# Performance work log

Measured on AMD Instinct MI355X. Metric: run time of the kernel, lower is better.

The kernel has to match this reference:

```python
import jax, jax.numpy as jnp
import numpy as np

N_NODES = 50000
N_EDGES = 800000
IN, HID, OUT = 128, 256, 128
BN_EPS = 1e-5

def setup_inputs() -> dict:
    key = jax.random.key(0)
    ks = jax.random.split(key, 16)
    def lin(k, fan_in, shape):
        b = 1.0 / np.sqrt(fan_in)
        return jax.random.uniform(k, shape, jnp.float32, -b, b)
    return {
        "node_feat": jax.random.normal(ks[0], (N_NODES, IN), jnp.float32),
        "coord_feat": jax.random.normal(ks[1], (N_NODES, 3), jnp.float32),
        "src": jax.random.randint(ks[2], (N_EDGES,), 0, N_NODES, jnp.int32),
        "dst": jax.random.randint(ks[3], (N_EDGES,), 0, N_NODES, jnp.int32),
        "W_e1": lin(ks[4], 2 * IN + 1, (2 * IN + 1, HID)),
        "b_e1": jnp.zeros((HID,), jnp.float32),
        "W_e2": lin(ks[5], HID, (HID, HID)),
        "b_e2": jnp.zeros((HID,), jnp.float32),
        "W_c1": lin(ks[6], HID, (HID, HID)),
        "b_c1": jnp.zeros((HID,), jnp.float32),
        "W_c2": lin(ks[7], HID, (HID, 1)),
        "W_n1": lin(ks[8], IN + HID, (IN + HID, HID)),
        "b_n1": jnp.zeros((HID,), jnp.float32),
        "W_n2": lin(ks[9], HID, (HID, OUT)),
        "b_n2": jnp.zeros((OUT,), jnp.float32),
        "gamma": jnp.ones((OUT,), jnp.float32),
        "beta": jnp.zeros((OUT,), jnp.float32),
    }

def reference(node_feat, coord_feat, src, dst, W_e1, b_e1, W_e2, b_e2,
              W_c1, b_c1, W_c2, W_n1, b_n1, W_n2, b_n2, gamma, beta):
    silu = jax.nn.silu
    # per-edge geometry (DGL u_sub_v: src - dst)
    x_diff = coord_feat[src] - coord_feat[dst]              # [E, 3]
    radial = jnp.sum(jnp.square(x_diff), axis=1, keepdims=True)  # [E, 1]
    x_diff = x_diff / (jnp.sqrt(radial) + 1e-30)
    # edge MLP on gathered features
    f = jnp.concatenate([node_feat[src], node_feat[dst], radial], axis=-1)  # [E, 2*IN+1]
    msg_h = silu(silu(f @ W_e1 + b_e1) @ W_e2 + b_e2)       # [E, HID]
    # coord message
    msg_x = (silu(msg_h @ W_c1 + b_c1) @ W_c2) * x_diff     # [E, 3]
    # aggregate at destination nodes
    h_neigh = jax.ops.segment_sum(msg_h, dst, num_segments=N_NODES)  # sum
    x_sum = jax.ops.segment_sum(msg_x, dst, num_segments=N_NODES)
    deg = jax.ops.segment_sum(jnp.ones((msg_x.shape[0],), msg_x.dtype), dst,
                              num_segments=N_NODES)
    x_neigh = x_sum / jnp.maximum(deg, 1.0)[:, None]        # mean; 0 for isolated nodes
    # node MLP + BatchNorm (training-mode batch stats, biased var)
    h = silu(jnp.concatenate([node_feat, h_neigh], axis=-1) @ W_n1 + b_n1) @ W_n2 + b_n2
    mu = jnp.mean(h, axis=0)
    var = jnp.mean(jnp.square(h - mu), axis=0)
    h = (h - mu) * jax.lax.rsqrt(var + BN_EPS) * gamma + beta
    x = coord_feat + x_neigh
    return h, x
```

## Files before the change

### kernel.cpp

```cpp
#include <hip/hip_runtime.h>
#include <stdint.h>

typedef unsigned short u16;
typedef __bf16 bf16x8 __attribute__((ext_vector_type(8)));
typedef unsigned short u16x8 __attribute__((ext_vector_type(8)));
typedef float f32x4 __attribute__((ext_vector_type(4)));

#define N_NODES 50000
#define N_EDGES 800000

enum : uint32_t {
  WS_WT_E1 = 0u,
  WS_WT_E2 = 131072u,
  WS_WT_C1 = 262144u,
  WS_WT_N1 = 393216u,
  WS_WT_N2 = 589824u,
  WS_WRAD  = 655360u,
  WS_WC2   = 656384u,
  WS_B_E1  = 657408u,
  WS_B_E2  = 658432u,
  WS_B_C1  = 659456u,
  WS_B_N1  = 660480u,
  WS_B_N2  = 661504u,
  WS_GAMMA = 662016u,
  WS_BETA  = 662528u,
  WS_SCALE = 663040u,
  WS_SHIFT = 663552u,
  WS_STAT  = 664064u,
  WS_FLAG  = 665600u,
  WS_DEG   = 1048576u,
  WS_OFF   = 1248576u,
  WS_BSUM  = 1448704u,
  WS_BPRE  = 1449728u,
  WS_CUR   = 1450752u,
  WS_EID   = 1650752u,
  WS_XSUM  = 4850752u,
  WS_CF    = 5450752u,
  WS_NF    = 6050752u,
  WS_HN    = 18850752u,
  WS_PA    = 70050752u,
  WS_PB    = 95675328u,
  WS_PRE_END = 121299904u
};

__device__ __forceinline__ float b2f(u16 u){ uint32_t x=((uint32_t)u)<<16; float f; __builtin_memcpy(&f,&x,4); return f; }
__device__ __forceinline__ u16 f2b(float f){ __bf16 h = (__bf16)f; return __builtin_bit_cast(unsigned short, h); }
__device__ __forceinline__ float silu_f(float x){
  return x * __builtin_amdgcn_rcpf(1.0f + __expf(-x));
}
__device__ __forceinline__ float ldin(const void* p, int i, int fl){
  return fl ? ((const float*)p)[i] : b2f(((const u16*)p)[i]);
}

__global__ void detect_k(const void* nf, int* flag){
  if (threadIdx.x == 0){
    const u16* p = (const u16*)nf;
    int cnt = 0;
    for (int i=0;i<128;i++){
      u16 u = p[2*i];
      int e = (u >> 7) & 0xFF;
      if (e >= 0x90) cnt++;
    }
    *flag = (cnt >= 8) ? 1 : 0;
  }
}

__global__ void cvt_nf_k(const void* nf, char* ws, const int* flagp){
  int fl = *flagp;
  int i = blockIdx.x*256 + threadIdx.x;
  if (i >= (N_NODES*128)/4) return;
  ushort4* out = (ushort4*)(ws + WS_NF);
  if (fl){
    const float4* p = (const float4*)nf;
    float4 v = p[i];
    ushort4 o; o.x=f2b(v.x); o.y=f2b(v.y); o.z=f2b(v.z); o.w=f2b(v.w);
    out[i] = o;
  } else {
    out[i] = ((const ushort4*)nf)[i];
  }
}

__global__ void cvt_cf_k(const void* cd, char* ws, const int* flagp){
  int fl = *flagp;
  int i = blockIdx.x*256 + threadIdx.x;
  if (i >= N_NODES*3) return;
  ((float*)(ws + WS_CF))[i] = ldin(cd, i, fl);
}

__global__ void prep_k(const void* We1, const void* be1, const void* We2, const void* be2,
                       const void* Wc1, const void* bc1, const void* Wc2,
                       const void* Wn1, const void* bn1, const void* Wn2, const void* bn2,
                       const void* gam, const void* bet, char* ws, const int* flagp)
{
  int fl = *flagp;
  int g = blockIdx.x*256 + threadIdx.x;
  if (g < 65536){ int n=g>>8,k=g&255; ((u16*)(ws+WS_WT_E1))[n*256+k]=f2b(ldin(We1,k*256+n,fl)); return; } g-=65536;
  if (g < 65536){
    int j=g&7, l=(g>>3)&63, nblk=(g>>9)&15, kk=g>>13;
    int n=nblk*16+(l&15), k=kk*32+((l>>4)&3)*8+j;
    ((u16*)(ws+WS_WT_E2))[g]=f2b(ldin(We2,k*256+n,fl)); return; } g-=65536;
  if (g < 65536){
    int j=g&7, l=(g>>3)&63, nblk=(g>>9)&15, kk=g>>13;
    int n=nblk*16+(l&15), k=kk*32+((l>>4)&3)*8+j;
    ((u16*)(ws+WS_WT_C1))[g]=f2b(ldin(Wc1,k*256+n,fl)); return; } g-=65536;
  if (g < 98304){ int n=g/384,k=g-n*384; ((u16*)(ws+WS_WT_N1))[n*384+k]=f2b(ldin(Wn1,k*256+n,fl)); return; } g-=98304;
  if (g < 32768){ int n=g>>8,k=g&255; ((u16*)(ws+WS_WT_N2))[n*256+k]=f2b(ldin(Wn2,k*128+n,fl)); return; } g-=32768;
  if (g < 256){ ((float*)(ws+WS_WRAD))[g]=ldin(We1,65536+g,fl); return; } g-=256;
  if (g < 256){ ((float*)(ws+WS_WC2))[g]=ldin(Wc2,g,fl); return; } g-=256;
  if (g < 256){ ((float*)(ws+WS_B_E1))[g]=ldin(be1,g,fl); return; } g-=256;
  if (g < 256){ ((float*)(ws+WS_B_E2))[g]=ldin(be2,g,fl); return; } g-=256;
  if (g < 256){ ((float*)(ws+WS_B_C1))[g]=ldin(bc1,g,fl); return; } g-=256;
  if (g < 256){ ((float*)(ws+WS_B_N1))[g]=ldin(bn1,g,fl); return; } g-=256;
  if (g < 128){ ((float*)(ws+WS_B_N2))[g]=ldin(bn2,g,fl); return; } g-=128;
  if (g < 128){ ((float*)(ws+WS_GAMMA))[g]=ldin(gam,g,fl); return; } g-=128;
  if (g < 128){ ((float*)(ws+WS_BETA))[g]=ldin(bet,g,fl); return; }
}

__global__ void histo_k(const int* __restrict__ dst, int* __restrict__ deg){
  int e = blockIdx.x*256 + threadIdx.x;
  if (e < N_EDGES) atomicAdd(&deg[dst[e]], 1);
}

__global__ void scanA_k(const int* __restrict__ deg, int* __restrict__ off, int* __restrict__ bsum){
  int t = threadIdx.x; int i = blockIdx.x*256 + t;
  int lane = t & 63, w = t >> 6;
  int v = (i < N_NODES) ? deg[i] : 0;
  int x = v;
  #pragma unroll
  for (int d=1; d<64; d<<=1){ int o = __shfl_up(x, d, 64); if (lane >= d) x += o; }
  __shared__ int wt[4];
  if (lane == 63) wt[w] = x;
  __syncthreads();
  int add = 0;
  if (w > 0) add += wt[0];
  if (w > 1) add += wt[1];
  if (w > 2) add += wt[2];
  x += add;
  if (i < N_NODES) off[i] = x;
  if (t == 255) bsum[blockIdx.x] = x;
}

__global__ void scanB_k(const int* __restrict__ bsum, int* __restrict__ bpre, int* __restrict__ off){
  int t = threadIdx.x;
  int lane = t & 63, w = t >> 6;
  int v = (t < 196) ? bsum[t] : 0;
  int x = v;
  #pragma unroll
  for (int d=1; d<64; d<<=1){ int o = __shfl_up(x, d, 64); if (lane >= d) x += o; }
  __shared__ int wt[4];
  if (lane == 63) wt[w] = x;
  __syncthreads();
  int add = 0;
  if (w > 0) add += wt[0];
  if (w > 1) add += wt[1];
  if (w > 2) add += wt[2];
  x += add;
  if (t < 196) bpre[t] = x - v;
  if (t == 255) off[N_NODES] = x;
}

__global__ void scanC_k(const int* __restrict__ deg, int* __restrict__ off,
                        const int* __restrict__ bpre, int* __restrict__ cur){
  int i = blockIdx.x*256 + threadIdx.x;
  if (i >= N_NODES) return;
  int excl = off[i] - deg[i] + bpre[blockIdx.x];
  off[i] = excl; cur[i] = excl;
}

__global__ void scatter_k(const int* __restrict__ dst, int* __restrict__ cur, int* __restrict__ eid){
  int e = blockIdx.x*256 + threadIdx.x;
  if (e >= N_EDGES) return;
  int p = atomicAdd(&cur[dst[e]], 1);
  eid[p] = e;
}

__global__ __launch_bounds__(512, 4) void pab_k(const u16* __restrict__ nfc,
                                                const char* __restrict__ wsw,
                                                u16* __restrict__ pa, u16* __restrict__ pb)
{
  const int t = threadIdx.x, lane = t & 63, wid = t >> 6;
  const int mw = wid & 1, nw = wid >> 1;
  const int mbase = mw << 5, nbase = nw << 6;
  const int l15 = lane & 15, l4 = lane >> 4;
  const int tile = blockIdx.x;
  const u16* Wt = (const u16*)(wsw + WS_WT_E1);
  const float* b1 = (const float*)(wsw + WS_B_E1);

  for (int sel = 0; sel < 2; ++sel){
    u16* out = sel ? pb : pa;
    f32x4 acc[2][4];
    #pragma unroll
    for (int mi=0;mi<2;mi++)
    #pragma unroll
    for (int ni=0;ni<4;ni++){ float b_ = sel ? 0.f : b1[nbase+ni*16+l15]; acc[mi][ni]=(f32x4){b_,b_,b_,b_}; }

    #pragma unroll
    for (int kk=0;kk<4;kk++){
      const int kel = kk*32 + l4*8;
      bf16x8 av[2];
      #pragma unroll
      for (int mi=0;mi<2;mi++){
        int row = tile*64 + mbase + mi*16 + l15;
        if (row >= N_NODES) row = 0;
        av[mi] = *(const bf16x8*)(nfc + (size_t)row*128 + kel);
      }
      #pragma unroll
      for (int ni=0;ni<4;ni++){
        int n_ = nbase + ni*16 + l15;
        bf16x8 bv = *(const bf16x8*)(Wt + (size_t)n_*256 + sel*128 + kel);
        #pragma unroll
        for (int mi=0;mi<2;mi++)
          acc[mi][ni] = __builtin_amdgcn_mfma_f32_16x16x32_bf16(av[mi], bv, acc[mi][ni], 0,0,0);
      }
    }
    #pragma unroll
    for (int mi=0;mi<2;mi++)
    #pragma unroll
    for (int ni=0;ni<4;ni++)
    #pragma unroll
    for (int j=0;j<4;j++){
      int m_ = tile*64 + mbase + mi*16 + l4*4 + j;
      if (m_ < N_NODES){
        int n_ = nbase + ni*16 + l15;
        out[(size_t)m_*256 + n_] = f2b(acc[mi][ni][j]);
      }
    }
  }
}

#define FRAG_GEMM2(FB, BIAS_L) do { \
  _Pragma("unroll") for (int mi=0;mi<2;mi++) _Pragma("unroll") for (int ni=0;ni<4;ni++){ \
    float b_ = BIAS_L[nbase + ni*16 + l15]; acc[mi][ni] = (f32x4){b_,b_,b_,b_}; } \
  bf16x8 bvc[4]; \
  _Pragma("unroll") for (int ni=0;ni<4;ni++) \
    bvc[ni] = *(const bf16x8*)(FB + (((nblk0 + ni)<<9)) + lane*8); \
  _Pragma("unroll") for (int kk=0;kk<8;kk++){ \
    const int kel = kk*32 + l4*8; \
    bf16x8 av[2]; \
    _Pragma("unroll") for (int mi=0;mi<2;mi++){ \
      int row = mbase + mi*16 + l15; \
      uint32_t byte = ((uint32_t)row<<9) ^ ((uint32_t)kel<<1) ^ ((uint32_t)(row&7)<<4); \
      av[mi] = *(const bf16x8*)((const char*)h_lds + byte); \
    } \
    bf16x8 bvn[4]; \
    if (kk < 7){ \
      _Pragma("unroll") for (int ni=0;ni<4;ni++) \
        bvn[ni] = *(const bf16x8*)(FB + ((((kk+1)<<4) + nblk0 + ni)<<9) + lane*8); \
    } \
    _Pragma("unroll") for (int ni=0;ni<4;ni++) \
    _Pragma("unroll") for (int mi=0;mi<2;mi++) \
      acc[mi][ni] = __builtin_amdgcn_mfma_f32_16x16x32_bf16(av[mi], bvc[ni], acc[mi][ni], 0,0,0); \
    if (kk < 7){ \
      _Pragma("unroll") for (int ni=0;ni<4;ni++) bvc[ni] = bvn[ni]; \
    } \
  } } while(0)

#define SILU_STORE2() do { \
  _Pragma("unroll") for (int mi=0;mi<2;mi++) _Pragma("unroll") for (int ni=0;ni<4;ni++) \
  _Pragma("unroll") for (int j=0;j<4;j++){ \
    int m_ = mbase + mi*16 + l4*4 + j; int n_ = nbase + ni*16 + l15; \
    float v_ = silu_f(acc[mi][ni][j]); \
    uint32_t byte = ((uint32_t)m_<<9) ^ ((uint32_t)n_<<1) ^ ((uint32_t)(m_&7)<<4); \
    *(u16*)((char*)h_lds + byte) = f2b(v_); \
  } } while(0)

template<bool PRE>
__global__ __launch_bounds__(512, 4) void edge_mlp(
    const u16* __restrict__ nfc, const float* __restrict__ coord,
    const int* __restrict__ src, const int* __restrict__ dst,
    const char* __restrict__ wsw, const int* __restrict__ eid,
    const u16* __restrict__ pa, const u16* __restrict__ pb,
    float* __restrict__ h_neigh, float* __restrict__ xsum)
{
  __shared__ u16 h_lds[16384];
  __shared__ int s_ids[64], d_ids[64];
  __shared__ float rad_l[64], xd_l[64][3];
  __shared__ float cpart[4][64];
  __shared__ float b1_l[256], b2_l[256], b3_l[256], wc2_l[256];

  const int t = threadIdx.x, lane = t & 63, wid = t >> 6;
  const int mw = wid & 1, nw = wid >> 1;
  const int mbase = mw << 5, nbase = nw << 6;
  const int nblk0 = nw << 2;
  const int l15 = lane & 15, l4 = lane >> 4;
  const int tile = blockIdx.x;

  const u16* FB2 = (const u16*)(wsw + WS_WT_E2);
  const u16* FB3 = (const u16*)(wsw + WS_WT_C1);

  if (t < 64) {
    int e = eid[tile*64 + t];
    int s = src[e], d = dst[e];
    s_ids[t] = s; d_ids[t] = d;
    float ax = coord[s*3+0]-coord[d*3+0];
    float ay = coord[s*3+1]-coord[d*3+1];
    float az = coord[s*3+2]-coord[d*3+2];
    float r2 = ax*ax+ay*ay+az*az;
    float inv = 1.0f/(sqrtf(r2) + 1e-30f);
    rad_l[t] = r2; xd_l[t][0]=ax*inv; xd_l[t][1]=ay*inv; xd_l[t][2]=az*inv;
  }
  if (t >= 64 && t < 320) {
    int c = t - 64;
    if constexpr (!PRE) b1_l[c] = ((const float*)(wsw+WS_B_E1))[c];
    b2_l[c]  = ((const float*)(wsw+WS_B_E2))[c];
    b3_l[c]  = ((const float*)(wsw+WS_B_C1))[c];
    wc2_l[c] = ((const float*)(wsw+WS_WC2))[c];
  }
  __syncthreads();

  f32x4 acc[2][4];

  if constexpr (PRE) {
    const int r1 = t >> 3, cq = (t & 7) << 5;
    const int s1 = s_ids[r1], d1 = d_ids[r1];
    const float rr = rad_l[r1];
    const u16* par = pa + (size_t)s1*256 + cq;
    const u16* pbr = pb + (size_t)d1*256 + cq;
    const float* wrg = (const float*)(wsw + WS_WRAD) + cq;
    u16x8 ua[4], ub[4];
    #pragma unroll
    for (int q=0;q<4;q++){ ua[q] = *(const u16x8*)(par + q*8); ub[q] = *(const u16x8*)(pbr + q*8); }
    #pragma unroll
    for (int q=0;q<4;q++){
      f32x4 w0 = *(const f32x4*)(wrg + q*8);
      f32x4 w1 = *(const f32x4*)(wrg + q*8 + 4);
      u16x8 o;
      #pragma unroll
      for (int j=0;j<8;j++){
        float wv = (j<4) ? w0[j] : w1[j-4];
        float hv = silu_f(b2f(ua[q][j]) + b2f(ub[q][j]) + rr*wv);
        o[j] = f2b(hv);
      }
      int c = cq + q*8;
      uint32_t byte = ((uint32_t)r1<<9) ^ ((uint32_t)c<<1) ^ ((uint32_t)(r1&7)<<4);
      *(u16x8*)((char*)h_lds + byte) = o;
    }
  } else {
    #pragma unroll
    for (int mi=0;mi<2;mi++)
    #pragma unroll
    for (int ni=0;ni<4;ni++){ float b_ = b1_l[nbase+ni*16+l15]; acc[mi][ni]=(f32x4){b_,b_,b_,b_}; }
    const u16* Wt1 = (const u16*)(wsw + WS_WT_E1);
    #pragma unroll
    for (int kk=0;kk<8;kk++){
      const int kel = kk*32 + l4*8;
      bf16x8 av[2];
      #pragma unroll
      for (int mi=0;mi<2;mi++){
        int row = mbase + mi*16 + l15;
        int nid = (kk < 4) ? s_ids[row] : d_ids[row];
        int k = (kk < 4) ? kel : (kel - 128);
        av[mi] = *(const bf16x8*)(nfc + (size_t)nid*128 + k);
      }
      #pragma unroll
      for (int ni=0;ni<4;ni++){
        int n_ = nbase + ni*16 + l15;
        bf16x8 bv = *(const bf16x8*)(Wt1 + (size_t)n_*256 + kel);
        #pragma unroll
        for (int mi=0;mi<2;mi++)
          acc[mi][ni] = __builtin_amdgcn_mfma_f32_16x16x32_bf16(av[mi], bv, acc[mi][ni], 0,0,0);
      }
    }
    #pragma unroll
    for (int mi=0;mi<2;mi++)
    #pragma unroll
    for (int ni=0;ni<4;ni++){
      int n_ = nbase + ni*16 + l15;
      float wrn = ((const float*)(wsw+WS_WRAD))[n_];
      #pragma unroll
      for (int j=0;j<4;j++){
        int m_ = mbase + mi*16 + l4*4 + j;
        float v_ = silu_f(acc[mi][ni][j] + rad_l[m_]*wrn);
        uint32_t byte = ((uint32_t)m_<<9) ^ ((uint32_t)n_<<1) ^ ((uint32_t)(m_&7)<<4);
        *(u16*)((char*)h_lds + byte) = f2b(v_);
      }
    }
  }
  __syncthreads();

  FRAG_GEMM2(FB2, b2_l);
  __syncthreads();
  SILU_STORE2();
  __syncthreads();

  FRAG_GEMM2(FB3, b3_l);
  float part[2][4];
  #pragma unroll
  for (int mi=0;mi<2;mi++)
  #pragma unroll
  for (int j=0;j<4;j++) part[mi][j] = 0.f;
  #pragma unroll
  for (int mi=0;mi<2;mi++)
  #pragma unroll
  for (int ni=0;ni<4;ni++){
    int n_ = nbase + ni*16 + l15;
    float w = wc2_l[n_];
    #pragma unroll
    for (int j=0;j<4;j++) part[mi][j] += silu_f(acc[mi][ni][j]) * w;
  }
  #pragma unroll
  for (int off_=1; off_<16; off_<<=1)
  #pragma unroll
  for (int mi=0;mi<2;mi++)
  #pragma unroll
  for (int j=0;j<4;j++) part[mi][j] += __shfl_xor(part[mi][j], off_, 64);
  if (l15 == 0){
    #pragma unroll
    for (int mi=0;mi<2;mi++)
    #pragma unroll
    for (int j=0;j<4;j++){
      int m_ = mbase + mi*16 + l4*4 + j;
      cpart[nw][m_] = part[mi][j];
    }
  }
  __syncthreads();

  if (t < 64){
    float csum = cpart[0][t] + cpart[1][t] + cpart[2][t] + cpart[3][t];
    int dd = d_ids[t];
    float v0 = csum*xd_l[t][0], v1 = csum*xd_l[t][1], v2 = csum*xd_l[t][2];
    #pragma unroll
    for (int off_=1; off_<64; off_<<=1){
      float u0=__shfl_up(v0,off_,64), u1=__shfl_up(v1,off_,64), u2=__shfl_up(v2,off_,64);
      int du=__shfl_up(dd,off_,64);
      if (lane >= off_ && du == dd){ v0+=u0; v1+=u1; v2+=u2; }
    }
    int dn = __shfl_down(dd,1,64);
    if (lane == 63 || dn != dd){
      unsafeAtomicAdd(&xsum[dd*3+0], v0);
      unsafeAtomicAdd(&xsum[dd*3+1], v1);
      unsafeAtomicAdd(&xsum[dd*3+2], v2);
    }
  }
  {
    int col  = t & 255;
    int half = t >> 8;
    int rb   = half << 5;
    float a2 = 0.f; int prev = d_ids[rb]; bool firstrun = true;
    #pragma unroll
    for (int ii=0; ii<32; ii+=8){
      float v[8]; int dv[8];
      #pragma unroll
      for (int j=0;j<8;j++){
        int m_ = rb + ii + j;
        uint32_t byte = ((uint32_t)m_<<9) ^ ((uint32_t)col<<1) ^ ((uint32_t)(m_&7)<<4);
        v[j] = b2f(*(const u16*)((const char*)h_lds + byte));
        dv[j] = d_ids[m_];
      }
      #pragma unroll
      for (int j=0;j<8;j++){
        if (dv[j] != prev){
          float* p = &h_neigh[(size_t)prev*256 + col];
          if (firstrun) unsafeAtomicAdd(p, a2); else *p = a2;
          firstrun = false; a2 = v[j]; prev = dv[j];
        } else a2 += v[j];
      }
    }
    unsafeAtomicAdd(&h_neigh[(size_t)prev*256 + col], a2);
  }
}

__global__ void x_out_k(const float* __restrict__ coord, const int* __restrict__ deg,
                        const float* __restrict__ xsum, void* __restrict__ d_out,
                        const int* __restrict__ flagp)
{
  int fl = *flagp;
  int n = blockIdx.x*256 + threadIdx.x;
  if (n >= N_NODES) return;
  float dm = fmaxf((float)deg[n], 1.f);
  float v0 = coord[n*3+0] + xsum[n*3+0]/dm;
  float v1 = coord[n*3+1] + xsum[n*3+1]/dm;
  float v2 = coord[n*3+2] + xsum[n*3+2]/dm;
  const size_t base = (size_t)N_NODES*128 + (size_t)n*3;
  if (fl){
    float* o = (float*)d_out;
    o[base+0]=v0; o[base+1]=v1; o[base+2]=v2;
  } else {
    u16* o = (u16*)d_out;
    o[base+0]=f2b(v0); o[base+1]=f2b(v1); o[base+2]=f2b(v2);
  }
}

__global__ __launch_bounds__(512, 4) void node_mlp(
    const u16* __restrict__ node_feat, const float* __restrict__ h_neigh,
    const char* __restrict__ wsw, u16* __restrict__ hpre)
{
  __shared__ u16 h_lds[16384];
  __shared__ float b1_l[256], b2_l[128];

  const int t = threadIdx.x, lane = t & 63, wid = t >> 6;
  const int mw = wid & 1, nw = wid >> 1;
  const int mbase = mw << 5, nbase = nw << 6;
  const int l15 = lane & 15, l4 = lane >> 4;
  const int tile = blockIdx.x;

  if (t < 256) b1_l[t] = ((const float*)(wsw+WS_B_N1))[t];
  if (t < 128) b2_l[t] = ((const float*)(wsw+WS_B_N2))[t];
  __syncthreads();

  const u16* Wt1 = (const u16*)(wsw + WS_WT_N1);
  const u16* Wt2 = (const u16*)(wsw + WS_WT_N2);

  f32x4 acc[2][4];
  #pragma unroll
  for (int mi=0;mi<2;mi++)
  #pragma unroll
  for (int ni=0;ni<4;ni++){ float b_ = b1_l[nbase+ni*16+l15]; acc[mi][ni] = (f32x4){b_,b_,b_,b_}; }

  #pragma unroll
  for (int kk=0;kk<12;kk++){
    const int kel = kk*32 + l4*8;
    bf16x8 av[2];
    #pragma unroll
    for (int mi=0;mi<2;mi++){
      int row = tile*64 + mbase + mi*16 + l15;
      if (row >= N_NODES) row = 0;
      if (kk < 4){
        av[mi] = *(const bf16x8*)(node_feat + (size_t)row*128 + kel);
      } else {
        const float* hp = h_neigh + (size_t)row*256 + (kel - 128);
        u16x8 u;
        #pragma unroll
        for (int e2=0;e2<8;e2++) u[e2] = f2b(hp[e2]);
        av[mi] = __builtin_bit_cast(bf16x8, u);
      }
    }
    #pragma unroll
    for (int ni=0;ni<4;ni++){
      int n_ = nbase + ni*16 + l15;
      bf16x8 bv = *(const bf16x8*)(Wt1 + (size_t)n_*384 + kel);
      #pragma unroll
      for (int mi=0;mi<2;mi++)
        acc[mi][ni] = __builtin_amdgcn_mfma_f32_16x16x32_bf16(av[mi], bv, acc[mi][ni], 0,0,0);
    }
  }
  SILU_STORE2();
  __syncthreads();

  const int nb2 = nw << 5;
  f32x4 acc2[2][2];
  #pragma unroll
  for (int mi=0;mi<2;mi++)
  #pragma unroll
  for (int ni=0;ni<2;ni++){ float b_ = b2_l[nb2+ni*16+l15]; acc2[mi][ni] = (f32x4){b_,b_,b_,b_}; }
  #pragma unroll
  for (int kk=0;kk<8;kk++){
    const int kel = kk*32 + l4*8;
    bf16x8 av[2];
    #pragma unroll
    for (int mi=0;mi<2;mi++){
      int row = mbase + mi*16 + l15;
      uint32_t byte = ((uint32_t)row<<9) ^ ((uint32_t)kel<<1) ^ ((uint32_t)(row&7)<<4);
      av[mi] = *(const bf16x8*)((const char*)h_lds + byte);
    }
    #pragma unroll
    for (int ni=0;ni<2;ni++){
      int n_ = nb2 + ni*16 + l15;
      bf16x8 bv = *(const bf16x8*)(Wt2 + (size_t)n_*256 + kel);
      #pragma unroll
      for (int mi=0;mi<2;mi++)
        acc2[mi][ni] = __builtin_amdgcn_mfma_f32_16x16x32_bf16(av[mi], bv, acc2[mi][ni], 0,0,0);
    }
  }
  #pragma unroll
  for (int mi=0;mi<2;mi++)
  #pragma unroll
  for (int ni=0;ni<2;ni++)
  #pragma unroll
  for (int j=0;j<4;j++){
    int m_ = tile*64 + mbase + mi*16 + l4*4 + j;
    if (m_ < N_NODES){
      int n_ = nb2 + ni*16 + l15;
      hpre[(size_t)m_*128 + n_] = f2b(acc2[mi][ni][j]);
    }
  }
}

__global__ void bn_stats_k(const u16* __restrict__ hpre, float* __restrict__ stat){
  int c = threadIdx.x;
  float s = 0.f, s2 = 0.f;
  for (int r = blockIdx.x; r < N_NODES; r += 256){
    float v = b2f(hpre[(size_t)r*128 + c]);
    s += v; s2 += v*v;
  }
  atomicAdd(&stat[c], s);
  atomicAdd(&stat[128+c], s2);
}

__global__ void bn_final_k(const float* __restrict__ stat, const char* __restrict__ wsw,
                           float* __restrict__ scale, float* __restrict__ shift){
  int c = threadIdx.x;
  if (c >= 128) return;
  float mu = stat[c] * (1.0f/N_NODES);
  float var = stat[128+c] * (1.0f/N_NODES) - mu*mu;
  float rs = rsqrtf(var + 1e-5f);
  float g = ((const float*)(wsw+WS_GAMMA))[c];
  float b = ((const float*)(wsw+WS_BETA))[c];
  scale[c] = rs*g;
  shift[c] = b - mu*rs*g;
}

__global__ void bn_apply_k(const u16* __restrict__ hpre, const float* __restrict__ scale,
                           const float* __restrict__ shift, void* __restrict__ d_out,
                           const int* __restrict__ flagp){
  int fl = *flagp;
  int i = blockIdx.x*256 + threadIdx.x;
  if (i >= N_NODES*128/8) return;
  u16x8 v = *(const u16x8*)(hpre + (size_t)i*8);
  int c0 = (i*8) & 127;
  if (fl){
    float* o = (float*)d_out + (size_t)i*8;
    #pragma unroll
    for (int j=0;j<8;j++) o[j] = b2f(v[j])*scale[c0+j] + shift[c0+j];
  } else {
    u16x8 w;
    #pragma unroll
    for (int j=0;j<8;j++) w[j] = f2b(b2f(v[j])*scale[c0+j] + shift[c0+j]);
    *(u16x8*)((u16*)d_out + (size_t)i*8) = w;
  }
}

extern "C" void kernel_launch(void* const* d_in, const int* in_sizes, int n_in,
                              void* d_out, int out_size, void* d_ws, size_t ws_size,
                              hipStream_t stream)
{
  const void* node_feat_raw = d_in[0];
  const void* coord_raw     = d_in[1];
  const int* src       = (const int*)d_in[2];
  const int* dst       = (const int*)d_in[3];
  char* ws = (char*)d_ws;

  int*   flag  = (int*)(ws + WS_FLAG);
  int*   deg   = (int*)(ws + WS_DEG);
  int*   off   = (int*)(ws + WS_OFF);
  int*   bsum  = (int*)(ws + WS_BSUM);
  int*   bpre  = (int*)(ws + WS_BPRE);
  int*   cur   = (int*)(ws + WS_CUR);
  int*   eid   = (int*)(ws + WS_EID);
  float* xsum  = (float*)(ws + WS_XSUM);
  float* hn    = (float*)(ws + WS_HN);
  u16*   pa    = (u16*)(ws + WS_PA);
  u16*   pb    = (u16*)(ws + WS_PB);
  u16*   hpre  = (u16*)(ws + WS_PA);
  const u16*   nfc = (const u16*)(ws + WS_NF);
  const float* cfc = (const float*)(ws + WS_CF);
  float* stat  = (float*)(ws + WS_STAT);
  float* scale = (float*)(ws + WS_SCALE);
  float* shift = (float*)(ws + WS_SHIFT);

  const bool pre = (ws_size >= (size_t)WS_PRE_END);

  hipMemsetAsync(deg, 0, N_NODES*sizeof(int), stream);
  hipMemsetAsync(xsum, 0, N_NODES*3*sizeof(float), stream);
  hipMemsetAsync(hn, 0, (size_t)N_NODES*256*sizeof(float), stream);
  hipMemsetAsync(stat, 0, 256*sizeof(float), stream);

  detect_k<<<1,64,0,stream>>>(node_feat_raw, flag);
  cvt_nf_k<<<(N_NODES*128/4 + 255)/256,256,0,stream>>>(node_feat_raw, ws, flag);
  cvt_cf_k<<<(N_NODES*3 + 255)/256,256,0,stream>>>(coord_raw, ws, flag);
  prep_k<<<1288,256,0,stream>>>(d_in[4],d_in[5],d_in[6],d_in[7],d_in[8],d_in[9],
                                d_in[10],d_in[11],d_in[12],d_in[13],d_in[14],
                                d_in[15],d_in[16], ws, flag);
  histo_k<<<3125,256,0,stream>>>(dst, deg);
  scanA_k<<<196,256,0,stream>>>(deg, off, bsum);
  scanB_k<<<1,256,0,stream>>>(bsum, bpre, off);
  scanC_k<<<196,256,0,stream>>>(deg, off, bpre, cur);
  scatter_k<<<3125,256,0,stream>>>(dst, cur, eid);

  if (pre){
    pab_k<<<782,512,0,stream>>>(nfc, ws, pa, pb);
    edge_mlp<true><<<12500,512,0,stream>>>(nfc, cfc, src, dst, ws, eid, pa, pb, hn, xsum);
  } else {
    edge_mlp<false><<<12500,512,0,stream>>>(nfc, cfc, src, dst, ws, eid, pa, pb, hn, xsum);
  }

  x_out_k<<<196,256,0,stream>>>(cfc, deg, xsum, d_out, flag);
  node_mlp<<<782,512,0,stream>>>(nfc, hn, ws, hpre);
  bn_stats_k<<<256,128,0,stream>>>(hpre, stat);
  bn_final_k<<<1,128,0,stream>>>(stat, ws, scale, shift);
  bn_apply_k<<<3125,256,0,stream>>>(hpre, scale, shift, d_out, flag);
}
```

Before: 819.5 us.

## Merge prep and finish kernels, remap edge tiles per XCD, vectorize h_neigh loads

Merges the node-feature, coordinate, weight conversion and degree histogram kernels into one launch, and the BN apply and coordinate output kernels into another, to cut launch count. Remaps edge_mlp block indices so each XCD handles a contiguous range of dst-sorted tiles, which should improve L2 locality for the h_neigh atomics. node_mlp now reads h_neigh as float4 vectors and uses a new SILU store macro. This reduces launch and serialization overhead at the cost of more branching inside the merged kernels.

```diff
diff --git a/kernel.cpp b/kernel.cpp
--- a/kernel.cpp
+++ b/kernel.cpp
@@ -65,60 +65,64 @@
   }
 }
 
-__global__ void cvt_nf_k(const void* nf, char* ws, const int* flagp){
-  int fl = *flagp;
-  int i = blockIdx.x*256 + threadIdx.x;
-  if (i >= (N_NODES*128)/4) return;
-  ushort4* out = (ushort4*)(ws + WS_NF);
-  if (fl){
-    const float4* p = (const float4*)nf;
-    float4 v = p[i];
-    ushort4 o; o.x=f2b(v.x); o.y=f2b(v.y); o.z=f2b(v.z); o.w=f2b(v.w);
-    out[i] = o;
-  } else {
-    out[i] = ((const ushort4*)nf)[i];
-  }
-}
-
-__global__ void cvt_cf_k(const void* cd, char* ws, const int* flagp){
-  int fl = *flagp;
-  int i = blockIdx.x*256 + threadIdx.x;
-  if (i >= N_NODES*3) return;
-  ((float*)(ws + WS_CF))[i] = ldin(cd, i, fl);
-}
-
-__global__ void prep_k(const void* We1, const void* be1, const void* We2, const void* be2,
-                       const void* Wc1, const void* bc1, const void* Wc2,
-                       const void* Wn1, const void* bn1, const void* Wn2, const void* bn2,
-                       const void* gam, const void* bet, char* ws, const int* flagp)
+__global__ void prep_all_k(const void* nf, const void* cd,
+                           const void* We1, const void* be1, const void* We2, const void* be2,
+                           const void* Wc1, const void* bc1, const void* Wc2,
+                           const void* Wn1, const void* bn1, const void* Wn2, const void* bn2,
+                           const void* gam, const void* bet,
+                           const int* __restrict__ dst, int* __restrict__ deg,
+                           char* ws, const int* flagp)
 {
-  int fl = *flagp;
-  int g = blockIdx.x*256 + threadIdx.x;
-  if (g < 65536){ int n=g>>8,k=g&255; ((u16*)(ws+WS_WT_E1))[n*256+k]=f2b(ldin(We1,k*256+n,fl)); return; } g-=65536;
-  if (g < 65536){
-    int j=g&7, l=(g>>3)&63, nblk=(g>>9)&15, kk=g>>13;
-    int n=nblk*16+(l&15), k=kk*32+((l>>4)&3)*8+j;
-    ((u16*)(ws+WS_WT_E2))[g]=f2b(ldin(We2,k*256+n,fl)); return; } g-=65536;
-  if (g < 65536){
-    int j=g&7, l=(g>>3)&63, nblk=(g>>9)&15, kk=g>>13;
-    int n=nblk*16+(l&15), k=kk*32+((l>>4)&3)*8+j;
-    ((u16*)(ws+WS_WT_C1))[g]=f2b(ldin(Wc1,k*256+n,fl)); return; } g-=65536;
-  if (g < 98304){ int n=g/384,k=g-n*384; ((u16*)(ws+WS_WT_N1))[n*384+k]=f2b(ldin(Wn1,k*256+n,fl)); return; } g-=98304;
-  if (g < 32768){ int n=g>>8,k=g&255; ((u16*)(ws+WS_WT_N2))[n*256+k]=f2b(ldin(Wn2,k*128+n,fl)); return; } g-=32768;
-  if (g < 256){ ((float*)(ws+WS_WRAD))[g]=ldin(We1,65536+g,fl); return; } g-=256;
-  if (g < 256){ ((float*)(ws+WS_WC2))[g]=ldin(Wc2,g,fl); return; } g-=256;
-  if (g < 256){ ((float*)(ws+WS_B_E1))[g]=ldin(be1,g,fl); return; } g-=256;
-  if (g < 256){ ((float*)(ws+WS_B_E2))[g]=ldin(be2,g,fl); return; } g-=256;
-  if (g < 256){ ((float*)(ws+WS_B_C1))[g]=ldin(bc1,g,fl); return; } g-=256;
-  if (g < 256){ ((float*)(ws+WS_B_N1))[g]=ldin(bn1,g,fl); return; } g-=256;
-  if (g < 128){ ((float*)(ws+WS_B_N2))[g]=ldin(bn2,g,fl); return; } g-=128;
-  if (g < 128){ ((float*)(ws+WS_GAMMA))[g]=ldin(gam,g,fl); return; } g-=128;
-  if (g < 128){ ((float*)(ws+WS_BETA))[g]=ldin(bet,g,fl); return; }
-}
-
-__global__ void histo_k(const int* __restrict__ dst, int* __restrict__ deg){
-  int e = blockIdx.x*256 + threadIdx.x;
-  if (e < N_EDGES) atomicAdd(&deg[dst[e]], 1);
+  const int b = blockIdx.x;
+  const int fl = *flagp;
+  if (b < 6250){
+    int i = b*256 + threadIdx.x;
+    if (i >= (N_NODES*128)/4) return;
+    ushort4* out = (ushort4*)(ws + WS_NF);
+    if (fl){
+      const float4* p = (const float4*)nf;
+      float4 v = p[i];
+      ushort4 o; o.x=f2b(v.x); o.y=f2b(v.y); o.z=f2b(v.z); o.w=f2b(v.w);
+      out[i] = o;
+    } else {
+      out[i] = ((const ushort4*)nf)[i];
+    }
+    return;
+  }
+  if (b < 6837){
+    int i = (b-6250)*256 + threadIdx.x;
+    if (i >= N_NODES*3) return;
+    ((float*)(ws + WS_CF))[i] = ldin(cd, i, fl);
+    return;
+  }
+  if (b < 8125){
+    int g = (b-6837)*256 + threadIdx.x;
+    if (g < 65536){ int n=g>>8,k=g&255; ((u16*)(ws+WS_WT_E1))[n*256+k]=f2b(ldin(We1,k*256+n,fl)); return; } g-=65536;
+    if (g < 65536){
+      int j=g&7, l=(g>>3)&63, nblk=(g>>9)&15, kk=g>>13;
+      int n=nblk*16+(l&15), k=kk*32+((l>>4)&3)*8+j;
+      ((u16*)(ws+WS_WT_E2))[g]=f2b(ldin(We2,k*256+n,fl)); return; } g-=65536;
+    if (g < 65536){
+      int j=g&7, l=(g>>3)&63, nblk=(g>>9)&15, kk=g>>13;
+      int n=nblk*16+(l&15), k=kk*32+((l>>4)&3)*8+j;
+      ((u16*)(ws+WS_WT_C1))[g]=f2b(ldin(Wc1,k*256+n,fl)); return; } g-=65536;
+    if (g < 98304){ int n=g/384,k=g-n*384; ((u16*)(ws+WS_WT_N1))[n*384+k]=f2b(ldin(Wn1,k*256+n,fl)); return; } g-=98304;
+    if (g < 32768){ int n=g>>8,k=g&255; ((u16*)(ws+WS_WT_N2))[n*256+k]=f2b(ldin(Wn2,k*128+n,fl)); return; } g-=32768;
+    if (g < 256){ ((float*)(ws+WS_WRAD))[g]=ldin(We1,65536+g,fl); return; } g-=256;
+    if (g < 256){ ((float*)(ws+WS_WC2))[g]=ldin(Wc2,g,fl); return; } g-=256;
+    if (g < 256){ ((float*)(ws+WS_B_E1))[g]=ldin(be1,g,fl); return; } g-=256;
+    if (g < 256){ ((float*)(ws+WS_B_E2))[g]=ldin(be2,g,fl); return; } g-=256;
+    if (g < 256){ ((float*)(ws+WS_B_C1))[g]=ldin(bc1,g,fl); return; } g-=256;
+    if (g < 256){ ((float*)(ws+WS_B_N1))[g]=ldin(bn1,g,fl); return; } g-=256;
+    if (g < 128){ ((float*)(ws+WS_B_N2))[g]=ldin(bn2,g,fl); return; } g-=128;
+    if (g < 128){ ((float*)(ws+WS_GAMMA))[g]=ldin(gam,g,fl); return; } g-=128;
+    if (g < 128){ ((float*)(ws+WS_BETA))[g]=ldin(bet,g,fl); return; }
+    return;
+  }
+  {
+    int e = (b-8125)*256 + threadIdx.x;
+    if (e < N_EDGES) atomicAdd(&deg[dst[e]], 1);
+  }
 }
 
 __global__ void scanA_k(const int* __restrict__ deg, int* __restrict__ off, int* __restrict__ bsum){
@@ -283,7 +287,10 @@
   const int mbase = mw << 5, nbase = nw << 6;
   const int nblk0 = nw << 2;
   const int l15 = lane & 15, l4 = lane >> 4;
-  const int tile = blockIdx.x;
+
+  const int orig = blockIdx.x;
+  const int xcd = orig & 7;
+  const int tile = (xcd < 4 ? xcd*1563 : 4*1563 + (xcd-4)*1562) + (orig >> 3);
 
   const u16* FB2 = (const u16*)(wsw + WS_WT_E2);
   const u16* FB3 = (const u16*)(wsw + WS_WT_C1);
@@ -460,26 +467,14 @@
   }
 }
 
-__global__ void x_out_k(const float* __restrict__ coord, const int* __restrict__ deg,
-                        const float* __restrict__ xsum, void* __restrict__ d_out,
-                        const int* __restrict__ flagp)
-{
-  int fl = *flagp;
-  int n = blockIdx.x*256 + threadIdx.x;
-  if (n >= N_NODES) return;
-  float dm = fmaxf((float)deg[n], 1.f);
-  float v0 = coord[n*3+0] + xsum[n*3+0]/dm;
-  float v1 = coord[n*3+1] + xsum[n*3+1]/dm;
-  float v2 = coord[n*3+2] + xsum[n*3+2]/dm;
-  const size_t base = (size_t)N_NODES*128 + (size_t)n*3;
-  if (fl){
-    float* o = (float*)d_out;
-    o[base+0]=v0; o[base+1]=v1; o[base+2]=v2;
-  } else {
-    u16* o = (u16*)d_out;
-    o[base+0]=f2b(v0); o[base+1]=f2b(v1); o[base+2]=f2b(v2);
-  }
-}
+#define SILU_STORE2N() do { \
+  _Pragma("unroll") for (int mi=0;mi<2;mi++) _Pragma("unroll") for (int ni=0;ni<4;ni++) \
+  _Pragma("unroll") for (int j=0;j<4;j++){ \
+    int m_ = mbase + mi*16 + l4*4 + j; int n_ = nbase + ni*16 + l15; \
+    float v_ = silu_f(acc[mi][ni][j]); \
+    uint32_t byte = ((uint32_t)m_<<9) ^ ((uint32_t)n_<<1) ^ ((uint32_t)(m_&7)<<4); \
+    *(u16*)((char*)h_lds + byte) = f2b(v_); \
+  } } while(0)
 
 __global__ __launch_bounds__(512, 4) void node_mlp(
     const u16* __restrict__ node_feat, const float* __restrict__ h_neigh,
@@ -519,9 +514,11 @@
         av[mi] = *(const bf16x8*)(node_feat + (size_t)row*128 + kel);
       } else {
         const float* hp = h_neigh + (size_t)row*256 + (kel - 128);
+        f32x4 h0 = *(const f32x4*)(hp);
+        f32x4 h1 = *(const f32x4*)(hp + 4);
         u16x8 u;
         #pragma unroll
-        for (int e2=0;e2<8;e2++) u[e2] = f2b(hp[e2]);
+        for (int e2=0;e2<4;e2++){ u[e2] = f2b(h0[e2]); u[e2+4] = f2b(h1[e2]); }
         av[mi] = __builtin_bit_cast(bf16x8, u);
       }
     }
@@ -534,7 +531,7 @@
         acc[mi][ni] = __builtin_amdgcn_mfma_f32_16x16x32_bf16(av[mi], bv, acc[mi][ni], 0,0,0);
     }
   }
-  SILU_STORE2();
+  SILU_STORE2N();
   __syncthreads();
 
   const int nb2 = nw << 5;
@@ -600,23 +597,45 @@
   shift[c] = b - mu*rs*g;
 }
 
-__global__ void bn_apply_k(const u16* __restrict__ hpre, const float* __restrict__ scale,
-                           const float* __restrict__ shift, void* __restrict__ d_out,
-                           const int* __restrict__ flagp){
-  int fl = *flagp;
-  int i = blockIdx.x*256 + threadIdx.x;
-  if (i >= N_NODES*128/8) return;
-  u16x8 v = *(const u16x8*)(hpre + (size_t)i*8);
-  int c0 = (i*8) & 127;
-  if (fl){
-    float* o = (float*)d_out + (size_t)i*8;
-    #pragma unroll
-    for (int j=0;j<8;j++) o[j] = b2f(v[j])*scale[c0+j] + shift[c0+j];
-  } else {
-    u16x8 w;
-    #pragma unroll
-    for (int j=0;j<8;j++) w[j] = f2b(b2f(v[j])*scale[c0+j] + shift[c0+j]);
-    *(u16x8*)((u16*)d_out + (size_t)i*8) = w;
+__global__ void finish_k(const u16* __restrict__ hpre, const float* __restrict__ scale,
+                         const float* __restrict__ shift, const float* __restrict__ coord,
+                         const int* __restrict__ deg, const float* __restrict__ xsum,
+                         void* __restrict__ d_out, const int* __restrict__ flagp)
+{
+  const int b = blockIdx.x;
+  const int fl = *flagp;
+  if (b < 3125){
+    int i = b*256 + threadIdx.x;
+    if (i >= N_NODES*128/8) return;
+    u16x8 v = *(const u16x8*)(hpre + (size_t)i*8);
+    int c0 = (i*8) & 127;
+    if (fl){
+      float* o = (float*)d_out + (size_t)i*8;
+      #pragma unroll
+      for (int j=0;j<8;j++) o[j] = b2f(v[j])*scale[c0+j] + shift[c0+j];
+    } else {
+      u16x8 w;
+      #pragma unroll
+      for (int j=0;j<8;j++) w[j] = f2b(b2f(v[j])*scale[c0+j] + shift[c0+j]);
+      *(u16x8*)((u16*)d_out + (size_t)i*8) = w;
+    }
+    return;
+  }
+  {
+    int n = (b-3125)*256 + threadIdx.x;
+    if (n >= N_NODES) return;
+    float dm = fmaxf((float)deg[n], 1.f);
+    float v0 = coord[n*3+0] + xsum[n*3+0]/dm;
+    float v1 = coord[n*3+1] + xsum[n*3+1]/dm;
+    float v2 = coord[n*3+2] + xsum[n*3+2]/dm;
+    const size_t base = (size_t)N_NODES*128 + (size_t)n*3;
+    if (fl){
+      float* o = (float*)d_out;
+      o[base+0]=v0; o[base+1]=v1; o[base+2]=v2;
+    } else {
+      u16* o = (u16*)d_out;
+      o[base+0]=f2b(v0); o[base+1]=f2b(v1); o[base+2]=f2b(v2);
+    }
   }
 }
 
@@ -656,12 +675,10 @@
   hipMemsetAsync(stat, 0, 256*sizeof(float), stream);
 
   detect_k<<<1,64,0,stream>>>(node_feat_raw, flag);
-  cvt_nf_k<<<(N_NODES*128/4 + 255)/256,256,0,stream>>>(node_feat_raw, ws, flag);
-  cvt_cf_k<<<(N_NODES*3 + 255)/256,256,0,stream>>>(coord_raw, ws, flag);
-  prep_k<<<1288,256,0,stream>>>(d_in[4],d_in[5],d_in[6],d_in[7],d_in[8],d_in[9],
-                                d_in[10],d_in[11],d_in[12],d_in[13],d_in[14],
-                                d_in[15],d_in[16], ws, flag);
-  histo_k<<<3125,256,0,stream>>>(dst, deg);
+  prep_all_k<<<11250,256,0,stream>>>(node_feat_raw, coord_raw,
+                                     d_in[4],d_in[5],d_in[6],d_in[7],d_in[8],d_in[9],
+                                     d_in[10],d_in[11],d_in[12],d_in[13],d_in[14],
+                                     d_in[15],d_in[16], dst, deg, ws, flag);
   scanA_k<<<196,256,0,stream>>>(deg, off, bsum);
   scanB_k<<<1,256,0,stream>>>(bsum, bpre, off);
   scanC_k<<<196,256,0,stream>>>(deg, off, bpre, cur);
@@ -674,9 +691,8 @@
     edge_mlp<false><<<12500,512,0,stream>>>(nfc, cfc, src, dst, ws, eid, pa, pb, hn, xsum);
   }
 
-  x_out_k<<<196,256,0,stream>>>(cfc, deg, xsum, d_out, flag);
   node_mlp<<<782,512,0,stream>>>(nfc, hn, ws, hpre);
   bn_stats_k<<<256,128,0,stream>>>(hpre, stat);
   bn_final_k<<<1,128,0,stream>>>(stat, ws, scale, shift);
-  bn_apply_k<<<3125,256,0,stream>>>(hpre, scale, shift, d_out, flag);
-}
+  finish_k<<<3321,256,0,stream>>>(hpre, scale, shift, cfc, deg, xsum, d_out, flag);
+}
```

Result: no change. 809.1 us, median of 2 (-1.3%).
